# Kernel tuning notes

Hardware: AMD Instinct MI355X
Metric: run time of the kernel (lower is better)

Reference implementation:

```python
import jax, jax.numpy as jnp
import numpy as np

N = 50000      # nodes
E = 800000     # edges (avg degree 16)
IN_DIM = 64
EMB = 64
L = 4          # num_layer
BN_EPS = 1e-5


def setup_inputs() -> dict:
    key = jax.random.key(0)
    ks = jax.random.split(key, 8)
    s = 0.05
    return {
        "x": jax.random.normal(ks[0], (N, 1, IN_DIM), jnp.float32),
        "edge_index": jax.random.randint(ks[1], (2, E), 0, N, jnp.int32),
        "edge_attr": jax.random.normal(ks[2], (E, 3), jnp.float32),
        "edge_weight": jax.random.uniform(ks[3], (E,), jnp.float32),
        # atom encoder Linear(in_dim, emb)
        "ae_w": jax.random.normal(ks[4], (IN_DIM, EMB), jnp.float32) * s,
        "ae_b": jnp.zeros((EMB,), jnp.float32),
        # per-layer GIN MLP: Linear -> BN -> ReLU -> Linear (stacked over L)
        "W1": jax.random.normal(ks[5], (L, EMB, EMB), jnp.float32) * s,
        "b1": jnp.zeros((L, EMB), jnp.float32),
        "g1": jnp.ones((L, EMB), jnp.float32),
        "be1": jnp.zeros((L, EMB), jnp.float32),
        "W2": jax.random.normal(ks[6], (L, EMB, EMB), jnp.float32) * s,
        "b2": jnp.zeros((L, EMB), jnp.float32),
        # outer per-layer BatchNorm1d in GNN_node
        "g_out": jnp.ones((L, EMB), jnp.float32),
        "be_out": jnp.zeros((L, EMB), jnp.float32),
    }


def _bn(h, g, b):
    # BatchNorm1d, training mode: batch stats over node dim, biased variance
    m = h.mean(0)
    v = h.var(0)
    return (h - m) * jax.lax.rsqrt(v + BN_EPS) * g + b


def reference(x, edge_index, edge_attr, edge_weight,
              ae_w, ae_b, W1, b1, g1, be1, W2, b2, g_out, be_out):
    # atom encoder on x[:, 0] : [N, in_dim] -> [N, emb]
    h = x[:, 0] @ ae_w + ae_b
    src = edge_index[0]
    dst = edge_index[1]
    n = h.shape[0]
    num_layers = W1.shape[0]
    for l in range(num_layers):
        # MyPyGINConv (train_eps=False, eps=0): scatter-add of x_j * w_e, plus self term
        msg = h[src] * edge_weight[:, None]                      # [E, emb]
        agg = jax.ops.segment_sum(msg, dst, num_segments=n)      # [N, emb]
        out = agg + h                                            # (1+eps)*x_r, eps=0
        # conv MLP: Linear -> BN -> ReLU -> Linear
        out = jax.nn.relu(_bn(out @ W1[l] + b1[l], g1[l], be1[l]))
        out = out @ W2[l] + b2[l]
        # outer BN + ReLU (always applied for 'originalgin'); dropout p=0; residual
        out = jax.nn.relu(_bn(out, g_out[l], be_out[l]))
        h = out + h
    return h  # JK='last'
```

## Files before the change

### kernel.cpp

```cpp
#include <hip/hip_runtime.h>
#include <stdint.h>

#define EMB 64
#define BN_EPS 1e-5f
#define BSH 8
#define CHUNK 4096
#define TS 68

typedef short bfrag __attribute__((ext_vector_type(8)));
typedef float f32x4 __attribute__((ext_vector_type(4)));

#define IN_F32    0
#define IN_BF16   1
#define IN_BF16BN 2

struct SMM {
  float tb[64 * TS];
  float st[128];
  float scs[EMB], shs[EMB];
  unsigned short wb[4096];
};

__device__ __forceinline__ unsigned short f2b(float x) {
  unsigned u = __float_as_uint(x);
  u += 0x7FFFu + ((u >> 16) & 1u);
  return (unsigned short)(u >> 16);
}
__device__ __forceinline__ float b2f(unsigned short v) {
  return __uint_as_float(((unsigned)v) << 16);
}

__device__ __forceinline__ void enc_tile(SMM& sm, int tile,
    const float* x, const float* aewf, const float* bias,
    unsigned short* out16, int N) {
  const int tid = threadIdx.x;
  const int lane = tid & 63;
  const int wv = tid >> 6;
  const int r = wv >> 1;
  const int c0 = (wv & 1) * 2;
  const int m = lane & 15;
  const int quad = lane >> 4;
  const int node0 = tile * 64;

#pragma unroll
  for (int it = 0; it < 8; it++) {
    int idx = it * 512 + tid;
    int j = idx >> 6, k = idx & 63;
    sm.wb[idx] = f2b(aewf[k * EMB + j]);
  }
  __syncthreads();

  bfrag a0 = {0, 0, 0, 0, 0, 0, 0, 0}, a1 = {0, 0, 0, 0, 0, 0, 0, 0};
  const int arow = node0 + r * 16 + m;
  if (arow < N) {
    const float* af = x + (size_t)arow * EMB + quad * 8;
#pragma unroll
    for (int j = 0; j < 8; j++) {
      a0[j] = (short)f2b(af[j]);
      a1[j] = (short)f2b(af[32 + j]);
    }
  }
  f32x4 zz[2];
#pragma unroll
  for (int cc = 0; cc < 2; cc++) {
    const int c = c0 + cc;
    const unsigned short* bb = &sm.wb[(c * 16 + m) * EMB + quad * 8];
    bfrag b0 = *(const bfrag*)bb;
    bfrag b1 = *(const bfrag*)(bb + 32);
    f32x4 z = {0.f, 0.f, 0.f, 0.f};
    z = __builtin_amdgcn_mfma_f32_16x16x32_bf16(a0, b0, z, 0, 0, 0);
    z = __builtin_amdgcn_mfma_f32_16x16x32_bf16(a1, b1, z, 0, 0, 0);
    zz[cc] = z;
  }
#pragma unroll
  for (int cc = 0; cc < 2; cc++) {
    const int c = c0 + cc;
    float bj = bias[c * 16 + m];
#pragma unroll
    for (int reg = 0; reg < 4; reg++) {
      int row = r * 16 + quad * 4 + reg;
      float v = (node0 + row < N) ? (zz[cc][reg] + bj) : 0.f;
      sm.tb[row * TS + c * 16 + m] = v;
    }
  }
  __syncthreads();
  ushort4* o4 = (ushort4*)(out16 + (size_t)node0 * EMB);
#pragma unroll
  for (int it = 0; it < 2; it++) {
    int flat4 = it * 512 + tid;
    int nsub = flat4 >> 4;
    int c4 = flat4 & 15;
    if (node0 + nsub < N) {
      const float* s4 = sm.tb + nsub * TS + c4 * 4;
      ushort4 o;
      o.x = f2b(s4[0]); o.y = f2b(s4[1]);
      o.z = f2b(s4[2]); o.w = f2b(s4[3]);
      o4[flat4] = o;
    }
  }
}

__global__ void __launch_bounds__(512) k_enc_prep(
        const float* __restrict__ x, const float* __restrict__ ae_w,
        const float* __restrict__ ae_b,
        const float* __restrict__ W1, const float* __restrict__ W2,
        unsigned short* __restrict__ Wt16, int* __restrict__ hist_part,
        float* __restrict__ stats, const int* __restrict__ ei,
        unsigned short* __restrict__ hb16,
        int E, int L, int nstats, int ntiles, int nchunks, int N) {
  __shared__ SMM sm;
  if ((int)blockIdx.x < ntiles) {
    enc_tile(sm, blockIdx.x, x, ae_w, ae_b, hb16, N);
    return;
  }
  const int pb = blockIdx.x - ntiles;
  const int tid = threadIdx.x;
  int* lh = (int*)sm.tb;
  const int nw2 = 2 * L * EMB * EMB;
  for (int gid = pb * 512 + tid; gid < nw2; gid += nchunks * 512) {
    int mI = gid >> 12;
    int j = (gid >> 6) & 63;
    int k = gid & 63;
    const float* src = (mI < L) ? W1 + (size_t)mI * EMB * EMB
                                : W2 + (size_t)(mI - L) * EMB * EMB;
    Wt16[EMB * EMB + gid] = f2b(src[k * EMB + j]);
  }
  for (int i = pb * 512 + tid; i < nstats; i += nchunks * 512) stats[i] = 0.0f;
  if (tid < 256) lh[tid] = 0;
  __syncthreads();
  const int c0 = pb * CHUNK;
  const int cend = min(c0 + CHUNK, E);
  for (int e = c0 + tid; e < cend; e += 512)
    atomicAdd(&lh[((unsigned)ei[E + e]) >> BSH], 1);
  __syncthreads();
  if (tid < 256) hist_part[pb * 256 + tid] = lh[tid];
}

__global__ void __launch_bounds__(256) k_part(
        const int* __restrict__ ei, const float* __restrict__ ew,
        const int* __restrict__ hist_part, int* __restrict__ bbase,
        int2* __restrict__ eG, int E, int nchunks, int nb) {
  __shared__ int a[256], lbase[256], loff[256];
  const int t = threadIdx.x;
  const int c = blockIdx.x;
  int pre = 0, post = 0;
#pragma unroll 8
  for (int cc = 0; cc < c; cc++) pre += hist_part[cc * 256 + t];
#pragma unroll 8
  for (int cc = c; cc < nchunks; cc++) post += hist_part[cc * 256 + t];
  const int tot = pre + post;
  a[t] = tot;
  __syncthreads();
  for (int off = 1; off < 256; off <<= 1) {
    int x = (t >= off) ? a[t - off] : 0;
    __syncthreads();
    a[t] += x;
    __syncthreads();
  }
  int excl = a[t] - tot;
  lbase[t] = excl + pre;
  loff[t] = 0;
  if (c == 0 && t <= nb) bbase[t] = excl;
  __syncthreads();
  const int c0 = c * CHUNK;
#pragma unroll 4
  for (int i = 0; i < 16; i++) {
    int e = c0 + i * 256 + t;
    if (e < E) {
      int d = ei[E + e];
      int g = ((unsigned)d) >> BSH;
      int pk = ei[e] | ((d & 255) << 24);
      int pos = lbase[g] + atomicAdd(&loff[g], 1);
      eG[pos] = make_int2(pk, __float_as_int(ew[e]));
    }
  }
}

__global__ void __launch_bounds__(256) k_build(
        const int2* __restrict__ eG, const int* __restrict__ bbase,
        int* __restrict__ rowst, int* __restrict__ counts,
        int2* __restrict__ pairs, int N) {
  __shared__ int lcnt[256], a[256], lcur[256];
  const int t = threadIdx.x;
  const int b = blockIdx.x;
  const int e0 = bbase[b], e1 = bbase[b + 1];
  lcnt[t] = 0;
  __syncthreads();
  for (int i = e0 + t; i < e1; i += 256)
    atomicAdd(&lcnt[((unsigned)eG[i].x) >> 24], 1);
  __syncthreads();
  int v = lcnt[t];
  a[t] = v;
  __syncthreads();
  for (int off = 1; off < 256; off <<= 1) {
    int x = (t >= off) ? a[t - off] : 0;
    __syncthreads();
    a[t] += x;
    __syncthreads();
  }
  int excl = a[t] - v;
  lcur[t] = excl;
  int node = (b << BSH) + t;
  if (node < N) { rowst[node] = e0 + excl; counts[node] = v; }
  __syncthreads();
  for (int i = e0 + t; i < e1; i += 256) {
    int2 p = eG[i];
    int loc = ((unsigned)p.x) >> 24;
    int pos = e0 + atomicAdd(&lcur[loc], 1);
    pairs[pos] = make_int2(p.x & 0x00FFFFFF, p.y);
  }
}

__global__ void k_agg(const unsigned short* __restrict__ hb,
                      const int* __restrict__ rowst,
                      const int* __restrict__ counts, const int2* __restrict__ pairs,
                      unsigned short* __restrict__ out16, int N) {
  const int lane = threadIdx.x & 63;
  const int half = lane >> 5;
  const int col = lane & 31;
  int wave = (blockIdx.x * blockDim.x + threadIdx.x) >> 6;
  const int nwaves = (gridDim.x * blockDim.x) >> 6;
  for (int nA = wave; nA < N; nA += 2 * nwaves) {
    const int nB = nA + nwaves;
    const int uA = __builtin_amdgcn_readfirstlane(nA);
    const int uB = __builtin_amdgcn_readfirstlane(nB);
    const bool hasB = uB < N;
    int sA = rowst[uA], eA = sA + counts[uA];
    int sB = 0, eB = 0;
    if (hasB) { sB = rowst[uB]; eB = sB + counts[uB]; }
    float a0A[4] = {0, 0, 0, 0}, a1A[4] = {0, 0, 0, 0};
    float a0B[4] = {0, 0, 0, 0}, a1B[4] = {0, 0, 0, 0};
    for (int xA = sA, xB = sB; (xA < eA) | (xB < eB); xA += 8, xB += 8) {
      int2 pA[8], pB[8];
#pragma unroll
      for (int k = 0; k < 8; k++) {
        int ia = xA + k;
        pA[k] = pairs[ia < eA ? ia : 0];
      }
#pragma unroll
      for (int k = 0; k < 8; k++) {
        int ib = xB + k;
        pB[k] = pairs[ib < eB ? ib : 0];
      }
#pragma unroll
      for (int j = 0; j < 4; j++) {
        int2 pp = half ? pA[2 * j + 1] : pA[2 * j];
        bool ok = (xA + 2 * j + half) < eA;
        float w = ok ? __int_as_float(pp.y) : 0.f;
        unsigned v = *((const unsigned*)(hb + (size_t)pp.x * EMB) + col);
        a0A[j] = fmaf(w, b2f((unsigned short)(v & 0xFFFFu)), a0A[j]);
        a1A[j] = fmaf(w, b2f((unsigned short)(v >> 16)), a1A[j]);
      }
#pragma unroll
      for (int j = 0; j < 4; j++) {
        int2 pp = half ? pB[2 * j + 1] : pB[2 * j];
        bool ok = (xB + 2 * j + half) < eB;
        float w = ok ? __int_as_float(pp.y) : 0.f;
        unsigned v = *((const unsigned*)(hb + (size_t)pp.x * EMB) + col);
        a0B[j] = fmaf(w, b2f((unsigned short)(v & 0xFFFFu)), a0B[j]);
        a1B[j] = fmaf(w, b2f((unsigned short)(v >> 16)), a1B[j]);
      }
    }
    {
      float s0 = (a0A[0] + a0A[1]) + (a0A[2] + a0A[3]);
      float s1 = (a1A[0] + a1A[1]) + (a1A[2] + a1A[3]);
      s0 += __shfl_xor(s0, 32);
      s1 += __shfl_xor(s1, 32);
      float v0 = __shfl(s0, lane >> 1);
      float v1 = __shfl(s1, lane >> 1);
      float sum = ((lane & 1) ? v1 : v0) + b2f(hb[(size_t)uA * EMB + lane]);
      out16[(size_t)uA * EMB + lane] = f2b(sum);
    }
    if (hasB) {
      float s0 = (a0B[0] + a0B[1]) + (a0B[2] + a0B[3]);
      float s1 = (a1B[0] + a1B[1]) + (a1B[2] + a1B[3]);
      s0 += __shfl_xor(s0, 32);
      s1 += __shfl_xor(s1, 32);
      float v0 = __shfl(s0, lane >> 1);
      float v1 = __shfl(s1, lane >> 1);
      float sum = ((lane & 1) ? v1 : v0) + b2f(hb[(size_t)uB * EMB + lane]);
      out16[(size_t)uB * EMB + lane] = f2b(sum);
    }
  }
}

__global__ void k_aggbn(const unsigned short* __restrict__ u16,
                        const unsigned short* __restrict__ hold,
                        const float* __restrict__ st,
                        const float* __restrict__ g, const float* __restrict__ be,
                        const int* __restrict__ rowst,
                        const int* __restrict__ counts,
                        const int2* __restrict__ pairs,
                        unsigned short* __restrict__ hnew,
                        unsigned short* __restrict__ out16,
                        float invN, int N) {
  __shared__ float scs[EMB], shs[EMB];
  const int tid = threadIdx.x;
  if (tid < EMB) {
    float s1 = 0.f, s2 = 0.f;
#pragma unroll
    for (int k = 0; k < 8; k++) {
      s1 += st[k * 128 + tid];
      s2 += st[k * 128 + 64 + tid];
    }
    float mu = s1 * invN;
    float va = fmaf(s2, invN, -mu * mu);
    float rs = rsqrtf(va + BN_EPS);
    float sc = rs * g[tid];
    scs[tid] = sc;
    shs[tid] = fmaf(-mu, sc, be[tid]);
  }
  __syncthreads();
  const int lane = tid & 63;
  const int half = lane >> 5;
  const int col = lane & 31;
  const float sc0 = scs[2 * col], sc1 = scs[2 * col + 1];
  const float sh0 = shs[2 * col], sh1 = shs[2 * col + 1];
  const float scl = scs[lane], shl = shs[lane];
  int wave = (blockIdx.x * blockDim.x + tid) >> 6;
  const int nwaves = (gridDim.x * blockDim.x) >> 6;
  for (int n = wave; n < N; n += nwaves) {
    const int un = __builtin_amdgcn_readfirstlane(n);
    const int s = rowst[un];
    const int e = s + counts[un];
    float uu = b2f(u16[(size_t)un * EMB + lane]);
    float hh = b2f(hold[(size_t)un * EMB + lane]);
    float hn = fmaxf(0.f, fmaf(uu, scl, shl)) + hh;
    float a0[4] = {0, 0, 0, 0}, a1[4] = {0, 0, 0, 0};
    for (int x = s; x < e; x += 8) {
      int2 pp[8];
#pragma unroll
      for (int k = 0; k < 8; k++) {
        int i = x + k;
        pp[k] = pairs[i < e ? i : 0];
      }
#pragma unroll
      for (int j = 0; j < 4; j++) {
        int2 p = half ? pp[2 * j + 1] : pp[2 * j];
        bool ok = (x + 2 * j + half) < e;
        float w = ok ? __int_as_float(p.y) : 0.f;
        const size_t base = (size_t)p.x * EMB;
        unsigned vu = *((const unsigned*)(u16 + base) + col);
        unsigned vh = *((const unsigned*)(hold + base) + col);
        float h0 = fmaxf(0.f, fmaf(b2f((unsigned short)(vu & 0xFFFFu)), sc0, sh0))
                   + b2f((unsigned short)(vh & 0xFFFFu));
        float h1 = fmaxf(0.f, fmaf(b2f((unsigned short)(vu >> 16)), sc1, sh1))
                   + b2f((unsigned short)(vh >> 16));
        a0[j] = fmaf(w, h0, a0[j]);
        a1[j] = fmaf(w, h1, a1[j]);
      }
    }
    float s0 = (a0[0] + a0[1]) + (a0[2] + a0[3]);
    float s1 = (a1[0] + a1[1]) + (a1[2] + a1[3]);
    s0 += __shfl_xor(s0, 32);
    s1 += __shfl_xor(s1, 32);
    float v0 = __shfl(s0, lane >> 1);
    float v1 = __shfl(s1, lane >> 1);
    float sum = ((lane & 1) ? v1 : v0) + hn;
    out16[(size_t)un * EMB + lane] = f2b(sum);
    hnew[(size_t)un * EMB + lane] = f2b(hn);
  }
}

template <int INMODE, bool DO_STATS>
__global__ void __launch_bounds__(256) k_mmx(
        const void* __restrict__ in_v, const unsigned short* __restrict__ Wt,
        const float* __restrict__ bias, const float* __restrict__ stats,
        const float* __restrict__ g, const float* __restrict__ be, float invN,
        unsigned short* __restrict__ out16, float* __restrict__ st_out, int N) {
  __shared__ float tb[64 * TS];
  __shared__ float st_part[128];
  __shared__ float scs[EMB], shs[EMB];
  const int tid = threadIdx.x;
  const int lane = tid & 63;
  const int wv = tid >> 6;
  const int node0 = blockIdx.x * 64;
  const int m = lane & 15;
  const int quad = lane >> 4;

  if (DO_STATS && tid < 128) st_part[tid] = 0.f;
  if (INMODE == IN_BF16BN) {
    if (tid < EMB) {
      float s1 = 0.f, s2 = 0.f;
#pragma unroll
      for (int k = 0; k < 8; k++) {
        s1 += stats[k * 128 + tid];
        s2 += stats[k * 128 + 64 + tid];
      }
      float mm = s1 * invN;
      float va = fmaf(s2, invN, -mm * mm);
      float rs = rsqrtf(va + BN_EPS);
      float sc = rs * g[tid];
      scs[tid] = sc;
      shs[tid] = fmaf(-mm, sc, be[tid]);
    }
    __syncthreads();
  }

  const int arow = node0 + wv * 16 + m;
  bfrag a0 = {0, 0, 0, 0, 0, 0, 0, 0}, a1 = {0, 0, 0, 0, 0, 0, 0, 0};
  if (arow < N) {
    if (INMODE == IN_BF16) {
      const unsigned short* ab =
          (const unsigned short*)in_v + (size_t)arow * EMB + quad * 8;
      a0 = *(const bfrag*)ab;
      a1 = *(const bfrag*)(ab + 32);
    } else if (INMODE == IN_BF16BN) {
      const unsigned short* ab =
          (const unsigned short*)in_v + (size_t)arow * EMB + quad * 8;
      bfrag r0 = *(const bfrag*)ab;
      bfrag r1 = *(const bfrag*)(ab + 32);
#pragma unroll
      for (int j = 0; j < 8; j++) {
        int k0 = quad * 8 + j;
        float v0 = b2f((unsigned short)r0[j]);
        float v1 = b2f((unsigned short)r1[j]);
        v0 = fmaxf(0.f, fmaf(v0, scs[k0], shs[k0]));
        v1 = fmaxf(0.f, fmaf(v1, scs[k0 + 32], shs[k0 + 32]));
        a0[j] = (short)f2b(v0);
        a1[j] = (short)f2b(v1);
      }
    }
  }

  const unsigned short* bb = Wt + (size_t)m * EMB + quad * 8;
  f32x4 acc[4];
#pragma unroll
  for (int c = 0; c < 4; c++) {
    bfrag b0 = *(const bfrag*)(bb + c * 16 * EMB);
    bfrag b1 = *(const bfrag*)(bb + c * 16 * EMB + 32);
    f32x4 z = {0.f, 0.f, 0.f, 0.f};
    z = __builtin_amdgcn_mfma_f32_16x16x32_bf16(a0, b0, z, 0, 0, 0);
    z = __builtin_amdgcn_mfma_f32_16x16x32_bf16(a1, b1, z, 0, 0, 0);
    acc[c] = z;
  }

#pragma unroll
  for (int c = 0; c < 4; c++) {
    float bj = bias[c * 16 + m];
#pragma unroll
    for (int r = 0; r < 4; r++) {
      int row = wv * 16 + quad * 4 + r;
      float v = (node0 + row < N) ? (acc[c][r] + bj) : 0.f;
      tb[row * TS + c * 16 + m] = v;
    }
  }
  __syncthreads();

  if (DO_STATS) {
    float ssum = 0.f, ssq = 0.f;
#pragma unroll
    for (int i = 0; i < 16; i++) {
      float v = tb[(wv * 16 + i) * TS + lane];
      ssum += v;
      ssq = fmaf(v, v, ssq);
    }
    atomicAdd(&st_part[lane], ssum);
    atomicAdd(&st_part[64 + lane], ssq);
  }

  ushort4* o4 = (ushort4*)(out16 + (size_t)node0 * EMB);
#pragma unroll
  for (int it = 0; it < 4; it++) {
    int flat4 = it * 256 + tid;
    int nsub = flat4 >> 4;
    int c4 = flat4 & 15;
    if (node0 + nsub < N) {
      const float* s4 = tb + nsub * TS + c4 * 4;
      ushort4 o;
      o.x = f2b(s4[0]); o.y = f2b(s4[1]);
      o.z = f2b(s4[2]); o.w = f2b(s4[3]);
      o4[flat4] = o;
    }
  }

  if (DO_STATS) {
    __syncthreads();
    if (tid < 128)
      atomicAdd(&st_out[((unsigned)blockIdx.x & 7u) * 128 + tid], st_part[tid]);
  }
}

__global__ void k_bnres_last(const unsigned short* __restrict__ u16,
                             const float* __restrict__ st,
                             const float* __restrict__ g,
                             const float* __restrict__ be,
                             const unsigned short* __restrict__ hb16,
                             float* __restrict__ out32,
                             float invN, int total4) {
  __shared__ float scs[EMB], shs[EMB];
  const int tid = threadIdx.x;
  if (tid < EMB) {
    float s1 = 0.f, s2 = 0.f;
#pragma unroll
    for (int k = 0; k < 8; k++) {
      s1 += st[k * 128 + tid];
      s2 += st[k * 128 + 64 + tid];
    }
    float mm = s1 * invN;
    float va = fmaf(s2, invN, -mm * mm);
    float rs = rsqrtf(va + BN_EPS);
    float sc = rs * g[tid];
    scs[tid] = sc;
    shs[tid] = fmaf(-mm, sc, be[tid]);
  }
  __syncthreads();
  int stride = gridDim.x * blockDim.x;
  for (int i4 = blockIdx.x * blockDim.x + tid; i4 < total4; i4 += stride) {
    int c4 = i4 & 15;
    ushort4 uv = ((const ushort4*)u16)[i4];
    ushort4 hv = ((const ushort4*)hb16)[i4];
    float4 scv = *(const float4*)&scs[c4 * 4];
    float4 shv = *(const float4*)&shs[c4 * 4];
    float4 o;
    o.x = fmaxf(0.f, fmaf(b2f(uv.x), scv.x, shv.x)) + b2f(hv.x);
    o.y = fmaxf(0.f, fmaf(b2f(uv.y), scv.y, shv.y)) + b2f(hv.y);
    o.z = fmaxf(0.f, fmaf(b2f(uv.z), scv.z, shv.z)) + b2f(hv.z);
    o.w = fmaxf(0.f, fmaf(b2f(uv.w), scv.w, shv.w)) + b2f(hv.w);
    ((float4*)out32)[i4] = o;
  }
}

extern "C" void kernel_launch(void* const* d_in, const int* in_sizes, int n_in,
                              void* d_out, int out_size, void* d_ws, size_t ws_size,
                              hipStream_t stream) {
  const float* x     = (const float*)d_in[0];
  const int*   ei    = (const int*)d_in[1];
  const float* ew    = (const float*)d_in[3];
  const float* ae_w  = (const float*)d_in[4];
  const float* ae_b  = (const float*)d_in[5];
  const float* W1    = (const float*)d_in[6];
  const float* b1    = (const float*)d_in[7];
  const float* g1    = (const float*)d_in[8];
  const float* be1   = (const float*)d_in[9];
  const float* W2    = (const float*)d_in[10];
  const float* b2    = (const float*)d_in[11];
  const float* g_out = (const float*)d_in[12];
  const float* be_out= (const float*)d_in[13];

  const int N = in_sizes[0] / EMB;
  const int E = in_sizes[3];
  const int L = in_sizes[6] / (EMB * EMB);
  const float invN = 1.0f / (float)N;
  const int NBUCK = (N + 255) >> BSH;
  const int nchunks = (E + CHUNK - 1) / CHUNK;

  uintptr_t p = (uintptr_t)d_ws;
  auto alloc = [&](size_t bytes) -> void* {
    p = (p + 255) & ~(uintptr_t)255;
    void* r = (void*)p;
    p += bytes;
    return r;
  };
  unsigned short* hbA  = (unsigned short*)alloc((size_t)N * EMB * 2);
  unsigned short* hbB  = (unsigned short*)alloc((size_t)N * EMB * 2);
  unsigned short* a16  = (unsigned short*)alloc((size_t)N * EMB * 2);
  unsigned short* t16  = (unsigned short*)alloc((size_t)N * EMB * 2);
  unsigned short* u16  = (unsigned short*)alloc((size_t)N * EMB * 2);
  unsigned short* Wt16 = (unsigned short*)alloc((size_t)(1 + 2 * L) * EMB * EMB * 2);
  int*   counts= (int*)alloc((size_t)N * 4);
  int*   rowst = (int*)alloc((size_t)N * 4);
  int*   hist_part = (int*)alloc((size_t)nchunks * 256 * 4);
  int*   bbase = (int*)alloc(257 * 4);
  int2*  pairs = (int2*)alloc((size_t)E * 8);
  int2*  eG    = (int2*)alloc((size_t)E * 8);
  float* stats = (float*)alloc((size_t)L * 2 * 8 * 128 * 4);
  (void)ws_size; (void)n_in; (void)out_size;

  const int ntiles = (N + 63) / 64;
  const int nstats = L * 2 * 8 * 128;

  hipLaunchKernelGGL(k_enc_prep, dim3(ntiles + nchunks), dim3(512), 0, stream,
                     x, ae_w, ae_b, W1, W2, Wt16, hist_part, stats, ei,
                     hbA, E, L, nstats, ntiles, nchunks, N);
  hipLaunchKernelGGL(k_part, dim3(nchunks), dim3(256), 0, stream,
                     ei, ew, hist_part, bbase, eG, E, nchunks, NBUCK);
  hipLaunchKernelGGL(k_build, dim3(NBUCK), dim3(256), 0, stream,
                     eG, bbase, rowst, counts, pairs, N);

  unsigned short* hcur = hbA;
  unsigned short* hnxt = hbB;
  for (int l = 0; l < L; l++) {
    float* stats1 = stats + (size_t)(l * 2 + 0) * 1024;
    float* stats2 = stats + (size_t)(l * 2 + 1) * 1024;

    if (l == 0) {
      hipLaunchKernelGGL(k_agg, dim3(2048), dim3(256), 0, stream,
                         hcur, rowst, counts, pairs, a16, N);
    } else {
      float* stats2p = stats + (size_t)((l - 1) * 2 + 1) * 1024;
      hipLaunchKernelGGL(k_aggbn, dim3(2048), dim3(256), 0, stream,
                         u16, hcur, stats2p, g_out + (size_t)(l - 1) * EMB,
                         be_out + (size_t)(l - 1) * EMB, rowst, counts, pairs,
                         hnxt, a16, invN, N);
      unsigned short* tmp = hcur; hcur = hnxt; hnxt = tmp;
    }
    hipLaunchKernelGGL((k_mmx<IN_BF16, true>), dim3(ntiles), dim3(256), 0, stream,
                       a16, Wt16 + (size_t)(1 + l) * EMB * EMB, b1 + (size_t)l * EMB,
                       (const float*)nullptr, (const float*)nullptr,
                       (const float*)nullptr, 0.f, t16, stats1, N);
    hipLaunchKernelGGL((k_mmx<IN_BF16BN, true>), dim3(ntiles), dim3(256), 0, stream,
                       t16, Wt16 + (size_t)(1 + L + l) * EMB * EMB, b2 + (size_t)l * EMB,
                       stats1, g1 + (size_t)l * EMB, be1 + (size_t)l * EMB, invN,
                       u16, stats2, N);
  }
  hipLaunchKernelGGL(k_bnres_last, dim3(1024), dim3(256), 0, stream,
                     u16, stats + (size_t)((L - 1) * 2 + 1) * 1024,
                     g_out + (size_t)(L - 1) * EMB, be_out + (size_t)(L - 1) * EMB,
                     hcur, (float*)d_out, invN, N * 16);
}
```

Measured before the change: 360.0 us.

## Interleave pre-BN output and residual into one packed table for gathers

Stores the pre-BN layer output and the residual h as interleaved bf16 pairs in a single per-node table. Each edge gather then needs one 8-byte load instead of two separate 4-byte loads from different arrays, which cuts scattered memory transactions in the aggregation kernel. The aggregation kernel also processes two destination nodes per wave to raise memory-level parallelism. The cost is a wider table per node, strided partial writes from the encoder, matmul and aggregation kernels, and more registers per wave.

Result: slower. 391.0 us (+8.6%).

```diff
diff --git a/kernel.cpp b/kernel.cpp
--- a/kernel.cpp
+++ b/kernel.cpp
@@ -29,10 +29,14 @@
 __device__ __forceinline__ float b2f(unsigned short v) {
   return __uint_as_float(((unsigned)v) << 16);
 }
+__device__ __forceinline__ unsigned pk2(unsigned short a, unsigned short b) {
+  return (unsigned)a | ((unsigned)b << 16);
+}
+
 
 __device__ __forceinline__ void enc_tile(SMM& sm, int tile,
     const float* x, const float* aewf, const float* bias,
-    unsigned short* out16, int N) {
+    unsigned short* hb0, unsigned int* I0u, int N) {
   const int tid = threadIdx.x;
   const int lane = tid & 63;
   const int wv = tid >> 6;
@@ -84,7 +88,7 @@
     }
   }
   __syncthreads();
-  ushort4* o4 = (ushort4*)(out16 + (size_t)node0 * EMB);
+  ushort4* o4 = (ushort4*)(hb0 + (size_t)node0 * EMB);
 #pragma unroll
   for (int it = 0; it < 2; it++) {
     int flat4 = it * 512 + tid;
@@ -96,6 +100,9 @@
       o.x = f2b(s4[0]); o.y = f2b(s4[1]);
       o.z = f2b(s4[2]); o.w = f2b(s4[3]);
       o4[flat4] = o;
+      size_t base = (size_t)(node0 + nsub) * 64 + 4 * c4;
+      I0u[base + 1] = pk2(o.x, o.y);
+      I0u[base + 3] = pk2(o.z, o.w);
     }
   }
 }
@@ -106,11 +113,11 @@
         const float* __restrict__ W1, const float* __restrict__ W2,
         unsigned short* __restrict__ Wt16, int* __restrict__ hist_part,
         float* __restrict__ stats, const int* __restrict__ ei,
-        unsigned short* __restrict__ hb16,
+        unsigned short* __restrict__ hb0, unsigned int* __restrict__ I0u,
         int E, int L, int nstats, int ntiles, int nchunks, int N) {
   __shared__ SMM sm;
   if ((int)blockIdx.x < ntiles) {
-    enc_tile(sm, blockIdx.x, x, ae_w, ae_b, hb16, N);
+    enc_tile(sm, blockIdx.x, x, ae_w, ae_b, hb0, I0u, N);
     return;
   }
   const int pb = blockIdx.x - ntiles;
@@ -284,14 +291,13 @@
   }
 }
 
-__global__ void k_aggbn(const unsigned short* __restrict__ u16,
-                        const unsigned short* __restrict__ hold,
+__global__ void k_aggbn(const uint2* __restrict__ Isrc,
+                        unsigned int* __restrict__ IdstU,
                         const float* __restrict__ st,
                         const float* __restrict__ g, const float* __restrict__ be,
                         const int* __restrict__ rowst,
                         const int* __restrict__ counts,
                         const int2* __restrict__ pairs,
-                        unsigned short* __restrict__ hnew,
                         unsigned short* __restrict__ out16,
                         float invN, int N) {
   __shared__ float scs[EMB], shs[EMB];
@@ -319,55 +325,106 @@
   const float scl = scs[lane], shl = shs[lane];
   int wave = (blockIdx.x * blockDim.x + tid) >> 6;
   const int nwaves = (gridDim.x * blockDim.x) >> 6;
-  for (int n = wave; n < N; n += nwaves) {
-    const int un = __builtin_amdgcn_readfirstlane(n);
-    const int s = rowst[un];
-    const int e = s + counts[un];
-    float uu = b2f(u16[(size_t)un * EMB + lane]);
-    float hh = b2f(hold[(size_t)un * EMB + lane]);
-    float hn = fmaxf(0.f, fmaf(uu, scl, shl)) + hh;
-    float a0[4] = {0, 0, 0, 0}, a1[4] = {0, 0, 0, 0};
-    for (int x = s; x < e; x += 8) {
-      int2 pp[8];
+  for (int nA = wave; nA < N; nA += 2 * nwaves) {
+    const int nB = nA + nwaves;
+    const int uA = __builtin_amdgcn_readfirstlane(nA);
+    const int uB = __builtin_amdgcn_readfirstlane(nB);
+    const bool hasB = uB < N;
+    int sA = rowst[uA], eA = sA + counts[uA];
+    int sB = 0, eB = 0;
+    if (hasB) { sB = rowst[uB]; eB = sB + counts[uB]; }
+    uint2 qA = Isrc[(size_t)uA * 32 + (lane >> 1)];
+    unsigned suA = (lane & 1) ? (qA.x >> 16) : (qA.x & 0xFFFFu);
+    unsigned hoA = (lane & 1) ? (qA.y >> 16) : (qA.y & 0xFFFFu);
+    float hnA = fmaxf(0.f, fmaf(b2f((unsigned short)suA), scl, shl)) +
+                b2f((unsigned short)hoA);
+    float hnB = 0.f;
+    if (hasB) {
+      uint2 qB = Isrc[(size_t)uB * 32 + (lane >> 1)];
+      unsigned suB = (lane & 1) ? (qB.x >> 16) : (qB.x & 0xFFFFu);
+      unsigned hoB = (lane & 1) ? (qB.y >> 16) : (qB.y & 0xFFFFu);
+      hnB = fmaxf(0.f, fmaf(b2f((unsigned short)suB), scl, shl)) +
+            b2f((unsigned short)hoB);
+    }
+    float a0A[4] = {0, 0, 0, 0}, a1A[4] = {0, 0, 0, 0};
+    float a0B[4] = {0, 0, 0, 0}, a1B[4] = {0, 0, 0, 0};
+    for (int xA = sA, xB = sB; (xA < eA) | (xB < eB); xA += 8, xB += 8) {
+      int2 pA[8], pB[8];
 #pragma unroll
       for (int k = 0; k < 8; k++) {
-        int i = x + k;
-        pp[k] = pairs[i < e ? i : 0];
+        int ia = xA + k;
+        pA[k] = pairs[ia < eA ? ia : 0];
+      }
+#pragma unroll
+      for (int k = 0; k < 8; k++) {
+        int ib = xB + k;
+        pB[k] = pairs[ib < eB ? ib : 0];
       }
 #pragma unroll
       for (int j = 0; j < 4; j++) {
-        int2 p = half ? pp[2 * j + 1] : pp[2 * j];
-        bool ok = (x + 2 * j + half) < e;
+        int2 p = half ? pA[2 * j + 1] : pA[2 * j];
+        bool ok = (xA + 2 * j + half) < eA;
         float w = ok ? __int_as_float(p.y) : 0.f;
-        const size_t base = (size_t)p.x * EMB;
-        unsigned vu = *((const unsigned*)(u16 + base) + col);
-        unsigned vh = *((const unsigned*)(hold + base) + col);
-        float h0 = fmaxf(0.f, fmaf(b2f((unsigned short)(vu & 0xFFFFu)), sc0, sh0))
-                   + b2f((unsigned short)(vh & 0xFFFFu));
-        float h1 = fmaxf(0.f, fmaf(b2f((unsigned short)(vu >> 16)), sc1, sh1))
-                   + b2f((unsigned short)(vh >> 16));
-        a0[j] = fmaf(w, h0, a0[j]);
-        a1[j] = fmaf(w, h1, a1[j]);
-      }
-    }
-    float s0 = (a0[0] + a0[1]) + (a0[2] + a0[3]);
-    float s1 = (a1[0] + a1[1]) + (a1[2] + a1[3]);
-    s0 += __shfl_xor(s0, 32);
-    s1 += __shfl_xor(s1, 32);
-    float v0 = __shfl(s0, lane >> 1);
-    float v1 = __shfl(s1, lane >> 1);
-    float sum = ((lane & 1) ? v1 : v0) + hn;
-    out16[(size_t)un * EMB + lane] = f2b(sum);
-    hnew[(size_t)un * EMB + lane] = f2b(hn);
-  }
-}
-
-template <int INMODE, bool DO_STATS>
+        uint2 q = Isrc[(size_t)p.x * 32 + col];
+        float h0 = fmaxf(0.f, fmaf(b2f((unsigned short)(q.x & 0xFFFFu)), sc0, sh0))
+                   + b2f((unsigned short)(q.y & 0xFFFFu));
+        float h1 = fmaxf(0.f, fmaf(b2f((unsigned short)(q.x >> 16)), sc1, sh1))
+                   + b2f((unsigned short)(q.y >> 16));
+        a0A[j] = fmaf(w, h0, a0A[j]);
+        a1A[j] = fmaf(w, h1, a1A[j]);
+      }
+#pragma unroll
+      for (int j = 0; j < 4; j++) {
+        int2 p = half ? pB[2 * j + 1] : pB[2 * j];
+        bool ok = (xB + 2 * j + half) < eB;
+        float w = ok ? __int_as_float(p.y) : 0.f;
+        uint2 q = Isrc[(size_t)p.x * 32 + col];
+        float h0 = fmaxf(0.f, fmaf(b2f((unsigned short)(q.x & 0xFFFFu)), sc0, sh0))
+                   + b2f((unsigned short)(q.y & 0xFFFFu));
+        float h1 = fmaxf(0.f, fmaf(b2f((unsigned short)(q.x >> 16)), sc1, sh1))
+                   + b2f((unsigned short)(q.y >> 16));
+        a0B[j] = fmaf(w, h0, a0B[j]);
+        a1B[j] = fmaf(w, h1, a1B[j]);
+      }
+    }
+    {
+      float s0 = (a0A[0] + a0A[1]) + (a0A[2] + a0A[3]);
+      float s1 = (a1A[0] + a1A[1]) + (a1A[2] + a1A[3]);
+      s0 += __shfl_xor(s0, 32);
+      s1 += __shfl_xor(s1, 32);
+      float v0 = __shfl(s0, lane >> 1);
+      float v1 = __shfl(s1, lane >> 1);
+      float sum = ((lane & 1) ? v1 : v0) + hnA;
+      out16[(size_t)uA * EMB + lane] = f2b(sum);
+      float hA0 = __shfl(hnA, (lane & 31) * 2);
+      float hA1 = __shfl(hnA, (lane & 31) * 2 + 1);
+      if (lane < 32)
+        IdstU[(size_t)uA * 64 + lane * 2 + 1] = pk2(f2b(hA0), f2b(hA1));
+    }
+    if (hasB) {
+      float s0 = (a0B[0] + a0B[1]) + (a0B[2] + a0B[3]);
+      float s1 = (a1B[0] + a1B[1]) + (a1B[2] + a1B[3]);
+      s0 += __shfl_xor(s0, 32);
+      s1 += __shfl_xor(s1, 32);
+      float v0 = __shfl(s0, lane >> 1);
+      float v1 = __shfl(s1, lane >> 1);
+      float sum = ((lane & 1) ? v1 : v0) + hnB;
+      out16[(size_t)uB * EMB + lane] = f2b(sum);
+      float hB0 = __shfl(hnB, (lane & 31) * 2);
+      float hB1 = __shfl(hnB, (lane & 31) * 2 + 1);
+      if (lane < 32)
+        IdstU[(size_t)uB * 64 + lane * 2 + 1] = pk2(f2b(hB0), f2b(hB1));
+    }
+  }
+}
+
+template <int INMODE, bool DO_STATS, bool UOUT>
 __global__ void __launch_bounds__(256) k_mmx(
         const void* __restrict__ in_v, const unsigned short* __restrict__ Wt,
         const float* __restrict__ bias, const float* __restrict__ stats,
         const float* __restrict__ g, const float* __restrict__ be, float invN,
-        unsigned short* __restrict__ out16, float* __restrict__ st_out, int N) {
+        unsigned short* __restrict__ out16, unsigned int* __restrict__ outIu,
+        float* __restrict__ st_out, int N) {
   __shared__ float tb[64 * TS];
   __shared__ float st_part[128];
   __shared__ float scs[EMB], shs[EMB];
@@ -459,7 +516,6 @@
     atomicAdd(&st_part[64 + lane], ssq);
   }
 
-  ushort4* o4 = (ushort4*)(out16 + (size_t)node0 * EMB);
 #pragma unroll
   for (int it = 0; it < 4; it++) {
     int flat4 = it * 256 + tid;
@@ -467,10 +523,16 @@
     int c4 = flat4 & 15;
     if (node0 + nsub < N) {
       const float* s4 = tb + nsub * TS + c4 * 4;
-      ushort4 o;
-      o.x = f2b(s4[0]); o.y = f2b(s4[1]);
-      o.z = f2b(s4[2]); o.w = f2b(s4[3]);
-      o4[flat4] = o;
+      if (UOUT) {
+        size_t base = (size_t)(node0 + nsub) * 64 + 4 * c4;
+        outIu[base]     = pk2(f2b(s4[0]), f2b(s4[1]));
+        outIu[base + 2] = pk2(f2b(s4[2]), f2b(s4[3]));
+      } else {
+        ushort4 o;
+        o.x = f2b(s4[0]); o.y = f2b(s4[1]);
+        o.z = f2b(s4[2]); o.w = f2b(s4[3]);
+        ((ushort4*)(out16 + (size_t)node0 * EMB))[flat4] = o;
+      }
     }
   }
 
@@ -481,11 +543,10 @@
   }
 }
 
-__global__ void k_bnres_last(const unsigned short* __restrict__ u16,
+__global__ void k_bnres_last(const uint4* __restrict__ I4,
                              const float* __restrict__ st,
                              const float* __restrict__ g,
                              const float* __restrict__ be,
-                             const unsigned short* __restrict__ hb16,
                              float* __restrict__ out32,
                              float invN, int total4) {
   __shared__ float scs[EMB], shs[EMB];
@@ -508,15 +569,18 @@
   int stride = gridDim.x * blockDim.x;
   for (int i4 = blockIdx.x * blockDim.x + tid; i4 < total4; i4 += stride) {
     int c4 = i4 & 15;
-    ushort4 uv = ((const ushort4*)u16)[i4];
-    ushort4 hv = ((const ushort4*)hb16)[i4];
+    uint4 q = I4[i4];
     float4 scv = *(const float4*)&scs[c4 * 4];
     float4 shv = *(const float4*)&shs[c4 * 4];
     float4 o;
-    o.x = fmaxf(0.f, fmaf(b2f(uv.x), scv.x, shv.x)) + b2f(hv.x);
-    o.y = fmaxf(0.f, fmaf(b2f(uv.y), scv.y, shv.y)) + b2f(hv.y);
-    o.z = fmaxf(0.f, fmaf(b2f(uv.z), scv.z, shv.z)) + b2f(hv.z);
-    o.w = fmaxf(0.f, fmaf(b2f(uv.w), scv.w, shv.w)) + b2f(hv.w);
+    o.x = fmaxf(0.f, fmaf(b2f((unsigned short)(q.x & 0xFFFFu)), scv.x, shv.x))
+          + b2f((unsigned short)(q.y & 0xFFFFu));
+    o.y = fmaxf(0.f, fmaf(b2f((unsigned short)(q.x >> 16)), scv.y, shv.y))
+          + b2f((unsigned short)(q.y >> 16));
+    o.z = fmaxf(0.f, fmaf(b2f((unsigned short)(q.z & 0xFFFFu)), scv.z, shv.z))
+          + b2f((unsigned short)(q.w & 0xFFFFu));
+    o.w = fmaxf(0.f, fmaf(b2f((unsigned short)(q.z >> 16)), scv.w, shv.w))
+          + b2f((unsigned short)(q.w >> 16));
     ((float4*)out32)[i4] = o;
   }
 }
@@ -552,11 +616,11 @@
     p += bytes;
     return r;
   };
-  unsigned short* hbA  = (unsigned short*)alloc((size_t)N * EMB * 2);
-  unsigned short* hbB  = (unsigned short*)alloc((size_t)N * EMB * 2);
-  unsigned short* a16  = (unsigned short*)alloc((size_t)N * EMB * 2);
-  unsigned short* t16  = (unsigned short*)alloc((size_t)N * EMB * 2);
-  unsigned short* u16  = (unsigned short*)alloc((size_t)N * EMB * 2);
+  unsigned int* Itab0 = (unsigned int*)alloc((size_t)N * 64 * 4);
+  unsigned int* Itab1 = (unsigned int*)alloc((size_t)N * 64 * 4);
+  unsigned short* hb0 = (unsigned short*)alloc((size_t)N * EMB * 2);
+  unsigned short* a16 = (unsigned short*)alloc((size_t)N * EMB * 2);
+  unsigned short* t16 = (unsigned short*)alloc((size_t)N * EMB * 2);
   unsigned short* Wt16 = (unsigned short*)alloc((size_t)(1 + 2 * L) * EMB * EMB * 2);
   int*   counts= (int*)alloc((size_t)N * 4);
   int*   rowst = (int*)alloc((size_t)N * 4);
@@ -567,45 +631,48 @@
   float* stats = (float*)alloc((size_t)L * 2 * 8 * 128 * 4);
   (void)ws_size; (void)n_in; (void)out_size;
 
+  unsigned int* Itab[2] = {Itab0, Itab1};
   const int ntiles = (N + 63) / 64;
   const int nstats = L * 2 * 8 * 128;
 
   hipLaunchKernelGGL(k_enc_prep, dim3(ntiles + nchunks), dim3(512), 0, stream,
                      x, ae_w, ae_b, W1, W2, Wt16, hist_part, stats, ei,
-                     hbA, E, L, nstats, ntiles, nchunks, N);
+                     hb0, Itab[0], E, L, nstats, ntiles, nchunks, N);
   hipLaunchKernelGGL(k_part, dim3(nchunks), dim3(256), 0, stream,
                      ei, ew, hist_part, bbase, eG, E, nchunks, NBUCK);
   hipLaunchKernelGGL(k_build, dim3(NBUCK), dim3(256), 0, stream,
                      eG, bbase, rowst, counts, pairs, N);
 
-  unsigned short* hcur = hbA;
-  unsigned short* hnxt = hbB;
   for (int l = 0; l < L; l++) {
     float* stats1 = stats + (size_t)(l * 2 + 0) * 1024;
     float* stats2 = stats + (size_t)(l * 2 + 1) * 1024;
+    unsigned int* Icur = Itab[l & 1];
 
     if (l == 0) {
       hipLaunchKernelGGL(k_agg, dim3(2048), dim3(256), 0, stream,
-                         hcur, rowst, counts, pairs, a16, N);
+                         hb0, rowst, counts, pairs, a16, N);
     } else {
       float* stats2p = stats + (size_t)((l - 1) * 2 + 1) * 1024;
       hipLaunchKernelGGL(k_aggbn, dim3(2048), dim3(256), 0, stream,
-                         u16, hcur, stats2p, g_out + (size_t)(l - 1) * EMB,
-                         be_out + (size_t)(l - 1) * EMB, rowst, counts, pairs,
-                         hnxt, a16, invN, N);
-      unsigned short* tmp = hcur; hcur = hnxt; hnxt = tmp;
-    }
-    hipLaunchKernelGGL((k_mmx<IN_BF16, true>), dim3(ntiles), dim3(256), 0, stream,
-                       a16, Wt16 + (size_t)(1 + l) * EMB * EMB, b1 + (size_t)l * EMB,
-                       (const float*)nullptr, (const float*)nullptr,
-                       (const float*)nullptr, 0.f, t16, stats1, N);
-    hipLaunchKernelGGL((k_mmx<IN_BF16BN, true>), dim3(ntiles), dim3(256), 0, stream,
-                       t16, Wt16 + (size_t)(1 + L + l) * EMB * EMB, b2 + (size_t)l * EMB,
-                       stats1, g1 + (size_t)l * EMB, be1 + (size_t)l * EMB, invN,
-                       u16, stats2, N);
+                         (const uint2*)Itab[(l + 1) & 1], Icur, stats2p,
+                         g_out + (size_t)(l - 1) * EMB,
+                         be_out + (size_t)(l - 1) * EMB,
+                         rowst, counts, pairs, a16, invN, N);
+    }
+    hipLaunchKernelGGL((k_mmx<IN_BF16, true, false>), dim3(ntiles), dim3(256), 0,
+                       stream, a16, Wt16 + (size_t)(1 + l) * EMB * EMB,
+                       b1 + (size_t)l * EMB, (const float*)nullptr,
+                       (const float*)nullptr, (const float*)nullptr, 0.f,
+                       t16, (unsigned int*)nullptr, stats1, N);
+    hipLaunchKernelGGL((k_mmx<IN_BF16BN, true, true>), dim3(ntiles), dim3(256), 0,
+                       stream, t16, Wt16 + (size_t)(1 + L + l) * EMB * EMB,
+                       b2 + (size_t)l * EMB, stats1, g1 + (size_t)l * EMB,
+                       be1 + (size_t)l * EMB, invN,
+                       (unsigned short*)nullptr, Icur, stats2, N);
   }
   hipLaunchKernelGGL(k_bnres_last, dim3(1024), dim3(256), 0, stream,
-                     u16, stats + (size_t)((L - 1) * 2 + 1) * 1024,
+                     (const uint4*)Itab[(L - 1) & 1],
+                     stats + (size_t)((L - 1) * 2 + 1) * 1024,
                      g_out + (size_t)(L - 1) * EMB, be_out + (size_t)(L - 1) * EMB,
-                     hcur, (float*)d_out, invN, N * 16);
-}
+                     (float*)d_out, invN, N * 16);
+}
```
